# Kernel tuning notes

Measured on AMD Instinct MI355X. Metric: run time of the kernel, lower is better.

## Reference

```python
import jax, jax.numpy as jnp
import numpy as np

B, H, S, DK, DV = 4, 16, 8192, 128, 128

def setup_inputs() -> dict:
    key = jax.random.key(0)
    k1, k2, k3, k4 = jax.random.split(key, 4)
    return {
        "K": jax.random.normal(k1, (B, H, S, DK), dtype=jnp.float32),
        "V": jax.random.normal(k2, (B, H, S, DV), dtype=jnp.float32),
        "M": jax.random.normal(k3, (B, H, DK, DV), dtype=jnp.float32),
        "z": jax.random.uniform(k4, (B, H, DK), dtype=jnp.float32),
    }

def reference(K, V, M, z):
    # phi = ELU(K) + 1  (positive feature map)
    phi_K = jax.nn.elu(K) + 1.0                                   # (B,H,S,dk)
    V_existing = jnp.einsum('bhsk,bhkv->bhsv', phi_K, M)          # (B,H,S,dv)
    delta_M = jnp.einsum('bhsk,bhsv->bhkv', phi_K, V - V_existing)
    new_M = M + delta_M                                           # (B,H,dk,dv)
    new_z = z + phi_K.sum(axis=-2)                                # (B,H,dk)
    return new_M, new_z
```

## Files before the change

kernel.cpp:

```cpp
#include <hip/hip_runtime.h>

#define BH 64
#define SEQ 8192
#define DK 128
#define DV 128
#define CS 64
#define LR 72

typedef _Float16 f16;
typedef _Float16 f16x4 __attribute__((ext_vector_type(4)));
typedef _Float16 f16x8 __attribute__((ext_vector_type(8)));
typedef float f32x4 __attribute__((ext_vector_type(4)));

template <int NC, bool PARTIAL>
__global__ __launch_bounds__(512, 4) void delta_phase1(
    const float* __restrict__ Kg, const float* __restrict__ Vg,
    float* __restrict__ dstP,
    float* __restrict__ dstG,
    float* __restrict__ newZ)
{
  __shared__ f16 phi_lds[DK * LR];
  __shared__ f16 v_lds[DV * LR];

  constexpr int SC  = SEQ / NC;
  constexpr int NST = SC / CS;

  const int chunk = blockIdx.x;
  const int bh    = blockIdx.y;
  const int tid   = threadIdx.x;
  const int wave  = tid >> 6;
  const int lane  = tid & 63;
  const int l31   = lane & 31;
  const int lhi   = lane >> 5;
  const int f15_  = lane & 15;
  const int quad  = lane >> 4;

  const float* Kh = Kg + ((size_t)bh * SEQ + (size_t)chunk * SC) * DK;
  const float* Vh = Vg + ((size_t)bh * SEQ + (size_t)chunk * SC) * DV;

  f32x4 acc[8][2];
#pragma unroll
  for (int r = 0; r < 8; ++r)
#pragma unroll
    for (int c = 0; c < 2; ++c)
      acc[r][c] = (f32x4){0.f, 0.f, 0.f, 0.f};

  float zacc[4] = {0.f, 0.f, 0.f, 0.f};

  for (int st = 0; st < NST; ++st) {
    __syncthreads();
    const float* Ks = Kh + (size_t)st * CS * DK;
    const float* Vs = Vh + (size_t)st * CS * DV;
    const int srow = wave * 8 + lhi * 4;
#pragma unroll
    for (int fj = 0; fj < 4; ++fj) {
      const int feat = fj * 32 + l31;
      const float* kp = Ks + (size_t)srow * DK + feat;
      const float a0 = kp[0];
      const float a1 = kp[DK];
      const float a2 = kp[2 * DK];
      const float a3 = kp[3 * DK];
      const float p0 = a0 > 0.f ? a0 + 1.f : __expf(a0);
      const float p1 = a1 > 0.f ? a1 + 1.f : __expf(a1);
      const float p2 = a2 > 0.f ? a2 + 1.f : __expf(a2);
      const float p3 = a3 > 0.f ? a3 + 1.f : __expf(a3);
      zacc[fj] += (p0 + p1) + (p2 + p3);
      *(f16x4*)&phi_lds[feat * LR + srow] =
          (f16x4){(f16)p0, (f16)p1, (f16)p2, (f16)p3};
      const float* vp = Vs + (size_t)srow * DV + feat;
      *(f16x4*)&v_lds[feat * LR + srow] =
          (f16x4){(f16)vp[0], (f16)vp[DV], (f16)vp[2 * DV], (f16)vp[3 * DV]};
    }
    __syncthreads();
    const f16* bsrc  = (wave < 4) ? v_lds : phi_lds;
    const int  cbase = (wave < 4) ? wave * 32 : wave * 32 - 128;
#pragma unroll
    for (int ss = 0; ss < 2; ++ss) {
      const int sb = ss * 32 + quad * 8;
      f16x8 bfr[2];
#pragma unroll
      for (int c = 0; c < 2; ++c)
        bfr[c] = *(const f16x8*)&bsrc[(cbase + c * 16 + f15_) * LR + sb];
#pragma unroll
      for (int r = 0; r < 8; ++r) {
        const f16x8 afr = *(const f16x8*)&phi_lds[(r * 16 + f15_) * LR + sb];
        acc[r][0] = __builtin_amdgcn_mfma_f32_16x16x32_f16(afr, bfr[0], acc[r][0], 0, 0, 0);
        acc[r][1] = __builtin_amdgcn_mfma_f32_16x16x32_f16(afr, bfr[1], acc[r][1], 0, 0, 0);
      }
    }
  }

  if (PARTIAL) {
    const size_t pb = (size_t)(bh * NC + chunk) * (128 * 256);
#pragma unroll
    for (int r = 0; r < 8; ++r)
#pragma unroll
      for (int c = 0; c < 2; ++c) {
        const int col = wave * 32 + c * 16 + f15_;
#pragma unroll
        for (int q = 0; q < 4; ++q) {
          const int row = r * 16 + quad * 4 + q;
          dstP[pb + (size_t)row * 256 + col] = acc[r][c][q];
        }
      }
  } else {
    const size_t mb = (size_t)bh * DK * DV;
#pragma unroll
    for (int r = 0; r < 8; ++r)
#pragma unroll
      for (int c = 0; c < 2; ++c) {
        const int col = wave * 32 + c * 16 + f15_;
#pragma unroll
        for (int q = 0; q < 4; ++q) {
          const int row = r * 16 + quad * 4 + q;
          const float v = acc[r][c][q];
          if (col < DV)
            atomicAdd(&dstP[mb + (size_t)row * DV + col], v);
          else
            atomicAdd(&dstG[mb + (size_t)row * DK + (col - DV)], v);
        }
      }
  }
#pragma unroll
  for (int fj = 0; fj < 4; ++fj) {
    float v = zacc[fj];
    v += __shfl_xor(v, 32, 64);
    if (lhi == 0) atomicAdd(&newZ[bh * DK + fj * 32 + l31], v);
  }
}

__global__ __launch_bounds__(256) void delta_reduce(
    const float* __restrict__ Pp, const float* __restrict__ Mg,
    float* __restrict__ newM, float* __restrict__ Gred, int NC)
{
  const int ct  = blockIdx.x;
  const int bh  = blockIdx.y;
  const int tid = threadIdx.x;
  const int col = ct * 32 + (tid & 31);
  const int r0  = tid >> 5;

  float acc[16];
#pragma unroll
  for (int i = 0; i < 16; ++i) acc[i] = 0.f;

  const float* base = Pp + (size_t)(bh * NC) * 32768;
  for (int ch = 0; ch < NC; ++ch) {
    const float* p = base + (size_t)ch * 32768;
#pragma unroll
    for (int i = 0; i < 16; ++i)
      acc[i] += p[(size_t)(r0 + 8 * i) * 256 + col];
  }
  if (col < 128) {
#pragma unroll
    for (int i = 0; i < 16; ++i) {
      const int row = r0 + 8 * i;
      newM[(size_t)bh * 16384 + (size_t)row * 128 + col] =
          Mg[(size_t)bh * 16384 + (size_t)row * 128 + col] + acc[i];
    }
  } else {
#pragma unroll
    for (int i = 0; i < 16; ++i) {
      const int row = r0 + 8 * i;
      Gred[(size_t)bh * 16384 + (size_t)row * 128 + (col - 128)] = acc[i];
    }
  }
}

__global__ __launch_bounds__(256) void delta_gm(
    const float* __restrict__ Mg, const float* __restrict__ G, float* __restrict__ newM)
{
  __shared__ float Gs[64 * 129];
  __shared__ float Ms[DK * 32];
  const int sub = blockIdx.x;
  const int bh  = blockIdx.y;
  const int kh  = sub >> 2;
  const int vt  = sub & 3;
  const int tid = threadIdx.x;
  const size_t mb = (size_t)bh * DK * DV;

  for (int i = tid; i < 64 * DK; i += 256)
    Gs[(i >> 7) * 129 + (i & 127)] = G[mb + (size_t)(kh * 64 + (i >> 7)) * DK + (i & 127)];
  for (int i = tid; i < DK * 32; i += 256)
    Ms[i] = Mg[mb + (size_t)(i >> 5) * DV + vt * 32 + (i & 31)];
  __syncthreads();

  const int kl = tid >> 2;
  const int vs = (tid & 3) * 8;
  float a[8];
#pragma unroll
  for (int j = 0; j < 8; ++j) a[j] = 0.f;
  for (int kk = 0; kk < DK; ++kk) {
    const float g = Gs[kl * 129 + kk];
#pragma unroll
    for (int j = 0; j < 8; ++j) a[j] += g * Ms[kk * 32 + vs + j];
  }
  float* dst = &newM[mb + (size_t)(kh * 64 + kl) * DV + vt * 32 + vs];
#pragma unroll
  for (int j = 0; j < 8; ++j) dst[j] -= a[j];
}

extern "C" void kernel_launch(void* const* d_in, const int* in_sizes, int n_in,
                              void* d_out, int out_size, void* d_ws, size_t ws_size,
                              hipStream_t stream) {
  const float* Kg = (const float*)d_in[0];
  const float* Vg = (const float*)d_in[1];
  const float* Mg = (const float*)d_in[2];
  const float* zg = (const float*)d_in[3];
  float* out  = (float*)d_out;
  float* newM = out;
  float* newZ = out + (size_t)BH * DK * DV;

  const size_t gredF = (size_t)BH * DK * DK;
  const size_t need16 = ((size_t)BH * 16 * 32768 + gredF) * sizeof(float);
  const size_t need8  = ((size_t)BH * 8  * 32768 + gredF) * sizeof(float);

  hipMemcpyAsync(newZ, zg, sizeof(float) * (size_t)BH * DK,
                 hipMemcpyDeviceToDevice, stream);

  if (ws_size >= need16) {
    float* Pp   = (float*)d_ws;
    float* Gred = Pp + (size_t)BH * 16 * 32768;
    delta_phase1<16, true><<<dim3(16, BH), 512, 0, stream>>>(Kg, Vg, Pp, nullptr, newZ);
    delta_reduce<<<dim3(8, BH), 256, 0, stream>>>(Pp, Mg, newM, Gred, 16);
    delta_gm<<<dim3(8, BH), 256, 0, stream>>>(Mg, Gred, newM);
  } else if (ws_size >= need8) {
    float* Pp   = (float*)d_ws;
    float* Gred = Pp + (size_t)BH * 8 * 32768;
    delta_phase1<8, true><<<dim3(8, BH), 512, 0, stream>>>(Kg, Vg, Pp, nullptr, newZ);
    delta_reduce<<<dim3(8, BH), 256, 0, stream>>>(Pp, Mg, newM, Gred, 8);
    delta_gm<<<dim3(8, BH), 256, 0, stream>>>(Mg, Gred, newM);
  } else {
    float* Gws = (float*)d_ws;
    hipMemcpyAsync(newM, Mg, sizeof(float) * (size_t)BH * DK * DV,
                   hipMemcpyDeviceToDevice, stream);
    hipMemsetAsync(Gws, 0, sizeof(float) * gredF, stream);
    delta_phase1<16, false><<<dim3(16, BH), 512, 0, stream>>>(Kg, Vg, newM, Gws, newZ);
    delta_gm<<<dim3(8, BH), 256, 0, stream>>>(Mg, Gws, newM);
  }
}
```

Before: 587.9 us.

## Prefetch next K/V stage into registers and reduce sequence chunks to eight

Phase 1 now loads the next 64-row K/V stage into registers while the MFMA work for the current stage runs, so global load latency overlaps with compute. A second barrier at the end of each iteration keeps the LDS tiles from being overwritten too early. The 16-chunk split is removed and the 8-chunk path is always used, which halves the grid to 512 blocks and the partial-sum traffic but gives less parallelism. The 32 extra registers per thread may hurt occupancy under the 512x4 launch bound.

```diff
diff --git a/kernel.cpp b/kernel.cpp
--- a/kernel.cpp
+++ b/kernel.cpp
@@ -37,6 +37,7 @@
 
   const float* Kh = Kg + ((size_t)bh * SEQ + (size_t)chunk * SC) * DK;
   const float* Vh = Vg + ((size_t)bh * SEQ + (size_t)chunk * SC) * DV;
+  const int srow = wave * 8 + lhi * 4;
 
   f32x4 acc[8][2];
 #pragma unroll
@@ -47,19 +48,34 @@
 
   float zacc[4] = {0.f, 0.f, 0.f, 0.f};
 
+  float kr[16], vr[16];
+#define LOAD_STAGE(ST)                                              \
+  {                                                                 \
+    const float* Ks_ = Kh + (size_t)(ST) * CS * DK;                 \
+    const float* Vs_ = Vh + (size_t)(ST) * CS * DV;                 \
+    _Pragma("unroll")                                               \
+    for (int fj = 0; fj < 4; ++fj) {                                \
+      const int feat_ = fj * 32 + l31;                              \
+      const float* kp_ = Ks_ + (size_t)srow * DK + feat_;           \
+      const float* vp_ = Vs_ + (size_t)srow * DV + feat_;           \
+      _Pragma("unroll")                                             \
+      for (int j = 0; j < 4; ++j) {                                 \
+        kr[fj * 4 + j] = kp_[(size_t)j * DK];                       \
+        vr[fj * 4 + j] = vp_[(size_t)j * DV];                       \
+      }                                                             \
+    }                                                               \
+  }
+
+  LOAD_STAGE(0);
+
   for (int st = 0; st < NST; ++st) {
-    __syncthreads();
-    const float* Ks = Kh + (size_t)st * CS * DK;
-    const float* Vs = Vh + (size_t)st * CS * DV;
-    const int srow = wave * 8 + lhi * 4;
 #pragma unroll
     for (int fj = 0; fj < 4; ++fj) {
       const int feat = fj * 32 + l31;
-      const float* kp = Ks + (size_t)srow * DK + feat;
-      const float a0 = kp[0];
-      const float a1 = kp[DK];
-      const float a2 = kp[2 * DK];
-      const float a3 = kp[3 * DK];
+      const float a0 = kr[fj * 4 + 0];
+      const float a1 = kr[fj * 4 + 1];
+      const float a2 = kr[fj * 4 + 2];
+      const float a3 = kr[fj * 4 + 3];
       const float p0 = a0 > 0.f ? a0 + 1.f : __expf(a0);
       const float p1 = a1 > 0.f ? a1 + 1.f : __expf(a1);
       const float p2 = a2 > 0.f ? a2 + 1.f : __expf(a2);
@@ -67,11 +83,14 @@
       zacc[fj] += (p0 + p1) + (p2 + p3);
       *(f16x4*)&phi_lds[feat * LR + srow] =
           (f16x4){(f16)p0, (f16)p1, (f16)p2, (f16)p3};
-      const float* vp = Vs + (size_t)srow * DV + feat;
       *(f16x4*)&v_lds[feat * LR + srow] =
-          (f16x4){(f16)vp[0], (f16)vp[DV], (f16)vp[2 * DV], (f16)vp[3 * DV]};
+          (f16x4){(f16)vr[fj * 4 + 0], (f16)vr[fj * 4 + 1],
+                  (f16)vr[fj * 4 + 2], (f16)vr[fj * 4 + 3]};
     }
     __syncthreads();
+
+    if (st + 1 < NST) LOAD_STAGE(st + 1);
+
     const f16* bsrc  = (wave < 4) ? v_lds : phi_lds;
     const int  cbase = (wave < 4) ? wave * 32 : wave * 32 - 128;
 #pragma unroll
@@ -88,7 +107,9 @@
         acc[r][1] = __builtin_amdgcn_mfma_f32_16x16x32_f16(afr, bfr[1], acc[r][1], 0, 0, 0);
       }
     }
-  }
+    __syncthreads();
+  }
+#undef LOAD_STAGE
 
   if (PARTIAL) {
     const size_t pb = (size_t)(bh * NC + chunk) * (128 * 256);
@@ -211,19 +232,12 @@
   float* newZ = out + (size_t)BH * DK * DV;
 
   const size_t gredF = (size_t)BH * DK * DK;
-  const size_t need16 = ((size_t)BH * 16 * 32768 + gredF) * sizeof(float);
-  const size_t need8  = ((size_t)BH * 8  * 32768 + gredF) * sizeof(float);
+  const size_t need8 = ((size_t)BH * 8 * 32768 + gredF) * sizeof(float);
 
   hipMemcpyAsync(newZ, zg, sizeof(float) * (size_t)BH * DK,
                  hipMemcpyDeviceToDevice, stream);
 
-  if (ws_size >= need16) {
-    float* Pp   = (float*)d_ws;
-    float* Gred = Pp + (size_t)BH * 16 * 32768;
-    delta_phase1<16, true><<<dim3(16, BH), 512, 0, stream>>>(Kg, Vg, Pp, nullptr, newZ);
-    delta_reduce<<<dim3(8, BH), 256, 0, stream>>>(Pp, Mg, newM, Gred, 16);
-    delta_gm<<<dim3(8, BH), 256, 0, stream>>>(Mg, Gred, newM);
-  } else if (ws_size >= need8) {
+  if (ws_size >= need8) {
     float* Pp   = (float*)d_ws;
     float* Gred = Pp + (size_t)BH * 8 * 32768;
     delta_phase1<8, true><<<dim3(8, BH), 512, 0, stream>>>(Kg, Vg, Pp, nullptr, newZ);
@@ -234,7 +248,7 @@
     hipMemcpyAsync(newM, Mg, sizeof(float) * (size_t)BH * DK * DV,
                    hipMemcpyDeviceToDevice, stream);
     hipMemsetAsync(Gws, 0, sizeof(float) * gredF, stream);
-    delta_phase1<16, false><<<dim3(16, BH), 512, 0, stream>>>(Kg, Vg, newM, Gws, newZ);
+    delta_phase1<8, false><<<dim3(8, BH), 512, 0, stream>>>(Kg, Vg, newM, Gws, newZ);
     delta_gm<<<dim3(8, BH), 256, 0, stream>>>(Mg, Gws, newM);
   }
 }
```

New measurement: 565.2 us. 3.9% less time.
